# Kernel optimization log

Hardware: AMD Instinct MI355X
Metric: run time of the kernel (lower is better)

## Reference

```python
import jax, jax.numpy as jnp
import numpy as np

BS, D, L, H = 8, 256, 1024, 8
DK = D // H
EPS = 1e-8


def setup_inputs() -> dict:
    key = jax.random.key(0)
    ks = jax.random.split(key, 9)
    queries = jax.random.normal(ks[0], (BS, D, L), jnp.float32)
    keys = jax.random.normal(ks[1], (BS, D, L), jnp.float32)
    values = jax.random.normal(ks[2], (BS, D, L), jnp.float32)
    # binary float mask over positions, (bs, L, 1) as the module expects
    mask = (jax.random.uniform(ks[3], (BS, L, 1)) > 0.1).astype(jnp.float32)
    # grouped 1x1 conv weights: one (dk, dk) block per head (xavier-ish scale)
    wscale = np.sqrt(2.0 / (DK + DK)).astype(np.float32)
    Wq = jax.random.normal(ks[4], (H, DK, DK), jnp.float32) * wscale
    Wk = jax.random.normal(ks[5], (H, DK, DK), jnp.float32) * wscale
    Wv = jax.random.normal(ks[6], (H, DK, DK), jnp.float32) * wscale
    # full 1x1 conv projection
    Wp = jax.random.normal(ks[7], (D, D), jnp.float32) * np.sqrt(1.0 / D).astype(np.float32)
    bp = jnp.zeros((D,), jnp.float32)
    return {"queries": queries, "keys": keys, "values": values, "mask": mask,
            "Wq": Wq, "Wk": Wk, "Wv": Wv, "Wp": Wp, "bp": bp}


def _grouped_conv1x1(x, W):
    # x: (bs, D, L) viewed as (bs, H, dk, L); W: (H, dk_out, dk_in)
    bs, _, l = x.shape
    xh = x.reshape(bs, H, DK, l)
    return jnp.einsum('hij,bhjl->bhil', W, xh)  # (bs, H, dk, L)


def _masked_softmax(logits, mask4):
    # logits: (bs, H, L, L); mask4: (bs, 1, 1, L) -- faithful to module's custom softmax
    max_value = jax.lax.stop_gradient(jnp.max(logits * mask4, axis=-1, keepdims=True))
    z = (logits - max_value) * mask4
    m = jnp.exp(z) * mask4
    n = jnp.sum(m, axis=-1, keepdims=True)
    p_mask = mask4 * jnp.swapaxes(mask4, 2, 3)  # (bs, 1, L, L)
    return p_mask * (m / (n + EPS))


def reference(queries, keys, values, mask, Wq, Wk, Wv, Wp, bp):
    bs, c, l = queries.shape
    m = jnp.swapaxes(mask, 1, 2)          # (bs, 1, L)
    m4 = m[:, :, None, :]                  # (bs, 1, 1, L)
    q = _grouped_conv1x1(queries, Wq) * m4  # (bs, H, dk, L)
    k = _grouped_conv1x1(keys, Wk) * m4
    v = _grouped_conv1x1(values, Wv)
    # attn[b,h,d,e] = sum_c q[b,h,c,d] k[b,h,c,e]  (no 1/sqrt(dk) scaling, as in source)
    attn = jnp.einsum('bhcd,bhce->bhde', q, k)
    atn = _masked_softmax(attn, m4)
    # value[b,h,c,k] = sum_d atn[b,h,k,d] * (v*mask)[b,h,c,d]
    val = jnp.einsum('bhkd,bhcd->bhck', atn, v * m4)
    val = val.reshape(bs, c, l)
    out = jnp.einsum('ij,bjl->bil', Wp, val) + bp[None, :, None]
    return jnp.swapaxes(out * m, 1, 2)      # (bs, L, D)
```

## Files before the change

### kernel.cpp

```cpp
#include <hip/hip_runtime.h>
#include <math.h>


constexpr int cD  = 256;
constexpr int cL  = 1024;
constexpr int cH  = 8;
constexpr int cDK = 32;

typedef _Float16 f16;
typedef __attribute__((ext_vector_type(8))) _Float16 h8;
typedef __attribute__((ext_vector_type(4))) _Float16 h4;
typedef __attribute__((ext_vector_type(4))) float f4v;

__global__ __launch_bounds__(256, 4) void proj_qkv_kernel(
    const float* __restrict__ queries, const float* __restrict__ keys,
    const float* __restrict__ values, const float* __restrict__ mask,
    const float* __restrict__ Wq, const float* __restrict__ Wk,
    const float* __restrict__ Wv, f16* __restrict__ qp_h,
    f16* __restrict__ kp_h, f16* __restrict__ vp_h)
{
    const int t    = threadIdx.x;
    const int bid  = blockIdx.x;
    const int lt   = bid & 15;
    const int bh   = bid >> 4;
    const int h    = bh & 7;
    const int b    = bh >> 3;
    const int l0   = lt * 64;
    const int lane = t & 63, w = t >> 6, ln15 = lane & 15, lq = lane >> 4;
    const int l    = l0 + w * 16 + ln15;

    const float mk = mask[b * cL + l];
    const size_t xbase = ((size_t)(b * cD + h * cDK)) * cL + l;
    const int    wbase = h * cDK * cDK + lq * 8;

    const float* Xs[3] = {queries, keys, values};
    const float* Ws[3] = {Wq, Wk, Wv};
    f4v d0[3], d1[3];

    #pragma unroll
    for (int m = 0; m < 3; ++m) {
        const float* __restrict__ X = Xs[m];
        const float* __restrict__ W = Ws[m];
        h8 bx, a0, a1;
        #pragma unroll
        for (int i = 0; i < 8; ++i)
            bx[i] = (f16)X[xbase + (size_t)(lq * 8 + i) * cL];
        #pragma unroll
        for (int i = 0; i < 8; ++i) {
            a0[i] = (f16)W[wbase + ln15 * cDK + i];
            a1[i] = (f16)W[wbase + (16 + ln15) * cDK + i];
        }
        f4v z = {0.f, 0.f, 0.f, 0.f};
        d0[m] = __builtin_amdgcn_mfma_f32_16x16x32_f16(a0, bx, z, 0, 0, 0);
        d1[m] = __builtin_amdgcn_mfma_f32_16x16x32_f16(a1, bx, z, 0, 0, 0);
    }

    {
        const size_t qb = ((size_t)bh * cL + l) * cDK;
        h4 o0, o1;
        #pragma unroll
        for (int i = 0; i < 4; ++i) { o0[i] = (f16)d0[0][i]; o1[i] = (f16)d1[0][i]; }
        *reinterpret_cast<h4*>(&qp_h[qb + lq * 4])      = o0;
        *reinterpret_cast<h4*>(&qp_h[qb + 16 + lq * 4]) = o1;
    }
    {
        const size_t kb = ((size_t)bh * cL + l) * cDK;
        h4 o0, o1;
        #pragma unroll
        for (int i = 0; i < 4; ++i) {
            o0[i] = (f16)(d0[1][i] * mk);
            o1[i] = (f16)(d1[1][i] * mk);
        }
        *reinterpret_cast<h4*>(&kp_h[kb + lq * 4])      = o0;
        *reinterpret_cast<h4*>(&kp_h[kb + 16 + lq * 4]) = o1;
    }
    {
        const size_t vb = (size_t)bh * cDK * cL + l;
        #pragma unroll
        for (int i = 0; i < 4; ++i) {
            vp_h[vb + (size_t)(lq * 4 + i) * cL]      = (f16)d0[2][i];
            vp_h[vb + (size_t)(16 + lq * 4 + i) * cL] = (f16)d1[2][i];
        }
    }
}

__global__ __launch_bounds__(256, 5) void attn_kernel(
    const float* __restrict__ mask, const f16* __restrict__ qp_h,
    const f16* __restrict__ kp_h, const f16* __restrict__ vp_h,
    f16* __restrict__ val_h)
{
    __shared__ __align__(16) char smem[28672];
    f16* ks  = (f16*)smem;
    f16* vsb = (f16*)(smem + 10240);
    f16* pbf = (f16*)(smem + 19456);

    const int t     = threadIdx.x;
    const int bid   = blockIdx.x;
    const int strip = bid & 15;
    const int bh    = bid >> 4;
    const int b     = bh >> 3;
    const int r0    = strip * 64;
    const int lane  = t & 63;
    const int w     = t >> 6;
    const int ln15  = lane & 15;
    const int lq    = lane >> 4;

    const size_t kvbase = ((size_t)bh) * 32768;
    const int se = t >> 2, sb = (t & 3) * 8;
    const int vc = t >> 3, veb = (t & 7) * 8;

    const h8 qf = *reinterpret_cast<const h8*>(
        &qp_h[((size_t)bh * cL + r0 + w * 16 + ln15) * cDK + lq * 8]);

    {
        h8 kh = *reinterpret_cast<const h8*>(&kp_h[kvbase + se * 32 + sb]);
        *reinterpret_cast<h8*>(&ks[se * 40 + sb]) = kh;
        h8 vv = *reinterpret_cast<const h8*>(&vp_h[kvbase + vc * 1024 + veb]);
        *reinterpret_cast<h8*>(&vsb[vc * 72 + veb]) = vv;
    }

    f4v o0 = {0.f, 0.f, 0.f, 0.f}, o1 = {0.f, 0.f, 0.f, 0.f};
    float mo = -INFINITY, lrp = 0.f;
    const int prow  = (w * 16 + ln15) * 72;
    const int vsoff = ln15 * 72 + lq * 8;

    for (int et = 0; et < 16; ++et) {
        __syncthreads();
        const int pp = et & 1;
        const bool pre = (et < 15);
        h8 khp, vvp;
        if (pre) {
            const int e0n = (et + 1) * 64;
            khp = *reinterpret_cast<const h8*>(&kp_h[kvbase + (e0n + se) * 32 + sb]);
            vvp = *reinterpret_cast<const h8*>(&vp_h[kvbase + vc * 1024 + e0n + veb]);
        }
        float4 mk4[4];
        #pragma unroll
        for (int es = 0; es < 4; ++es)
            mk4[es] = *reinterpret_cast<const float4*>(
                &mask[b * cL + et * 64 + es * 16 + lq * 4]);

        f4v sA[4];
        #pragma unroll
        for (int es = 0; es < 4; ++es) {
            const h8 kf = *reinterpret_cast<const h8*>(
                &ks[pp * 2560 + (es * 16 + ln15) * 40 + lq * 8]);
            f4v z = {0.f, 0.f, 0.f, 0.f};
            sA[es] = __builtin_amdgcn_mfma_f32_16x16x32_f16(kf, qf, z, 0, 0, 0);
        }

        float tm = fmaxf(fmaxf(fmaxf(sA[0][0], sA[0][1]), fmaxf(sA[0][2], sA[0][3])),
                   fmaxf(fmaxf(fmaxf(sA[1][0], sA[1][1]), fmaxf(sA[1][2], sA[1][3])),
                   fmaxf(fmaxf(fmaxf(sA[2][0], sA[2][1]), fmaxf(sA[2][2], sA[2][3])),
                         fmaxf(fmaxf(sA[3][0], sA[3][1]), fmaxf(sA[3][2], sA[3][3])))));
        tm = fmaxf(tm, __shfl_xor(tm, 16));
        tm = fmaxf(tm, __shfl_xor(tm, 32));
        const float mn = fmaxf(mo, tm);
        const float al = __expf(mo - mn);
        mo = mn;
        o0[0] *= al; o0[1] *= al; o0[2] *= al; o0[3] *= al;
        o1[0] *= al; o1[1] *= al; o1[2] *= al; o1[3] *= al;

        float ps = 0.f;
        #pragma unroll
        for (int es = 0; es < 4; ++es) {
            float p0 = mk4[es].x * __expf(sA[es][0] - mn);
            float p1 = mk4[es].y * __expf(sA[es][1] - mn);
            float p2 = mk4[es].z * __expf(sA[es][2] - mn);
            float p3 = mk4[es].w * __expf(sA[es][3] - mn);
            ps += (p0 + p1) + (p2 + p3);
            h4 pk; pk[0] = (f16)p0; pk[1] = (f16)p1; pk[2] = (f16)p2; pk[3] = (f16)p3;
            *reinterpret_cast<h4*>(&pbf[prow + es * 16 + lq * 4]) = pk;
        }
        lrp = lrp * al + ps;

        #pragma unroll
        for (int ch = 0; ch < 2; ++ch) {
            h8 pf  = *reinterpret_cast<const h8*>(&pbf[prow + ch * 32 + lq * 8]);
            h8 va0 = *reinterpret_cast<const h8*>(&vsb[pp * 2304 + vsoff + ch * 32]);
            h8 va1 = *reinterpret_cast<const h8*>(&vsb[pp * 2304 + vsoff + ch * 32 + 1152]);
            o0 = __builtin_amdgcn_mfma_f32_16x16x32_f16(va0, pf, o0, 0, 0, 0);
            o1 = __builtin_amdgcn_mfma_f32_16x16x32_f16(va1, pf, o1, 0, 0, 0);
        }

        if (pre) {
            *reinterpret_cast<h8*>(&ks[(pp ^ 1) * 2560 + se * 40 + sb]) = khp;
            *reinterpret_cast<h8*>(&vsb[(pp ^ 1) * 2304 + vc * 72 + veb]) = vvp;
        }
    }

    {
        float lr = lrp;
        lr += __shfl_xor(lr, 16);
        lr += __shfl_xor(lr, 32);
        const float linv = 1.0f / (lr + 1e-8f);
        const int h = bh & 7;
        const size_t obase = ((size_t)(b * cL + r0 + w * 16 + ln15)) * cD + h * cDK;
        h4 q0, q1;
        #pragma unroll
        for (int i = 0; i < 4; ++i) {
            q0[i] = (f16)(o0[i] * linv);
            q1[i] = (f16)(o1[i] * linv);
        }
        *reinterpret_cast<h4*>(&val_h[obase + lq * 4])      = q0;
        *reinterpret_cast<h4*>(&val_h[obase + 16 + lq * 4]) = q1;
    }
}

__global__ __launch_bounds__(256, 2) void outproj_kernel(
    const f16* __restrict__ val_h, const float* __restrict__ Wp,
    const float* __restrict__ bp, const float* __restrict__ mask,
    float* __restrict__ out)
{
    __shared__ __align__(16) f16 vt[64 * 264];
    __shared__ __align__(16) f16 wpb[64 * 264];
    __shared__ float mrow[64];

    const int t    = threadIdx.x;
    const int bid  = blockIdx.x;
    const int it   = bid & 3;
    const int lt   = (bid >> 2) & 15;
    const int b    = bid >> 6;
    const int l0   = lt * 64, i0 = it * 64;
    const int lane = t & 63, w = t >> 6, ln15 = lane & 15, lq = lane >> 4;

    {
        int row = t & 63, seg = (t >> 6) * 64;
        const f16* src = &val_h[((size_t)(b * cL + l0 + row)) * cD + seg];
        #pragma unroll
        for (int k = 0; k < 8; ++k)
            *reinterpret_cast<h8*>(&vt[row * 264 + seg + k * 8]) =
                *reinterpret_cast<const h8*>(src + k * 8);
    }
    {
        int row = t & 63, seg = (t >> 6) * 64;
        const float* src = &Wp[((size_t)(i0 + row)) * cD + seg];
        #pragma unroll
        for (int k = 0; k < 8; ++k) {
            float4 f0 = *reinterpret_cast<const float4*>(src + k * 8);
            float4 f1 = *reinterpret_cast<const float4*>(src + k * 8 + 4);
            h8 hv;
            hv[0] = (f16)f0.x; hv[1] = (f16)f0.y; hv[2] = (f16)f0.z; hv[3] = (f16)f0.w;
            hv[4] = (f16)f1.x; hv[5] = (f16)f1.y; hv[6] = (f16)f1.z; hv[7] = (f16)f1.w;
            *reinterpret_cast<h8*>(&wpb[row * 264 + seg + k * 8]) = hv;
        }
    }
    if (t < 64) mrow[t] = mask[b * cL + l0 + t];
    __syncthreads();

    f4v acc[4] = {{0.f, 0.f, 0.f, 0.f}, {0.f, 0.f, 0.f, 0.f},
                  {0.f, 0.f, 0.f, 0.f}, {0.f, 0.f, 0.f, 0.f}};
    #pragma unroll
    for (int kc = 0; kc < 8; ++kc) {
        h8 aA = *reinterpret_cast<const h8*>(&vt[(w * 16 + ln15) * 264 + kc * 32 + lq * 8]);
        #pragma unroll
        for (int ti = 0; ti < 4; ++ti) {
            h8 bB = *reinterpret_cast<const h8*>(&wpb[(ti * 16 + ln15) * 264 + kc * 32 + lq * 8]);
            acc[ti] = __builtin_amdgcn_mfma_f32_16x16x32_f16(aA, bB, acc[ti], 0, 0, 0);
        }
    }

    float mk[4];
    #pragma unroll
    for (int rg = 0; rg < 4; ++rg) mk[rg] = mrow[w * 16 + lq * 4 + rg];
    #pragma unroll
    for (int ti = 0; ti < 4; ++ti) {
        float bpv = bp[i0 + ti * 16 + ln15];
        #pragma unroll
        for (int rg = 0; rg < 4; ++rg) {
            int l = l0 + w * 16 + lq * 4 + rg;
            out[((size_t)(b * cL + l)) * cD + i0 + ti * 16 + ln15] =
                (acc[ti][rg] + bpv) * mk[rg];
        }
    }
}

extern "C" void kernel_launch(void* const* d_in, const int* in_sizes, int n_in,
                              void* d_out, int out_size, void* d_ws, size_t ws_size,
                              hipStream_t stream) {
    const float* queries = (const float*)d_in[0];
    const float* keys    = (const float*)d_in[1];
    const float* values  = (const float*)d_in[2];
    const float* mask    = (const float*)d_in[3];
    const float* Wq      = (const float*)d_in[4];
    const float* Wk      = (const float*)d_in[5];
    const float* Wv      = (const float*)d_in[6];
    const float* Wp      = (const float*)d_in[7];
    const float* bp      = (const float*)d_in[8];
    float* out = (float*)d_out;

    char* wsb = (char*)d_ws;
    f16* qp_h  = (f16*)(wsb);
    f16* kp_h  = (f16*)(wsb + (4u << 20));
    f16* vp_h  = (f16*)(wsb + (8u << 20));
    f16* val_h = (f16*)(wsb + (12u << 20));

    proj_qkv_kernel<<<dim3(1024), dim3(256), 0, stream>>>(
        queries, keys, values, mask, Wq, Wk, Wv, qp_h, kp_h, vp_h);
    attn_kernel<<<dim3(1024), dim3(256), 0, stream>>>(
        mask, qp_h, kp_h, vp_h, val_h);
    outproj_kernel<<<dim3(512), dim3(256), 0, stream>>>(val_h, Wp, bp, mask, out);
}
```

Before: 127.3 us.

## Stage projection weights in LDS, pre-convert Wp, use exp2 softmax, reorder attention blocks

The projection kernel now stages each head's fp16 Wq/Wk/Wv in shared memory instead of gathering them per thread from global memory. Extra blocks in the same kernel convert Wp to fp16 once, so the output projection can read val_h and wp_h straight from global memory with no LDS staging and a higher occupancy bound. Q is prescaled by log2(e) so the attention softmax can use exp2f. The attention block index is remapped so consecutive blocks cover different batch-head pairs. The risks are more uncoalesced or repeated global reads in outproj and a small fp16 rounding change from the scaling.

New measurement: 142.1 us. 1.12x slower.

```diff
diff --git a/kernel.cpp b/kernel.cpp
--- a/kernel.cpp
+++ b/kernel.cpp
@@ -6,6 +6,7 @@
 constexpr int cL  = 1024;
 constexpr int cH  = 8;
 constexpr int cDK = 32;
+constexpr float kLog2e = 1.44269504088896f;
 
 typedef _Float16 f16;
 typedef __attribute__((ext_vector_type(8))) _Float16 h8;
@@ -16,11 +17,23 @@
     const float* __restrict__ queries, const float* __restrict__ keys,
     const float* __restrict__ values, const float* __restrict__ mask,
     const float* __restrict__ Wq, const float* __restrict__ Wk,
-    const float* __restrict__ Wv, f16* __restrict__ qp_h,
-    f16* __restrict__ kp_h, f16* __restrict__ vp_h)
+    const float* __restrict__ Wv, const float* __restrict__ Wp,
+    f16* __restrict__ qp_h, f16* __restrict__ kp_h, f16* __restrict__ vp_h,
+    f16* __restrict__ wp_h)
 {
-    const int t    = threadIdx.x;
-    const int bid  = blockIdx.x;
+    const int t   = threadIdx.x;
+    const int bid = blockIdx.x;
+
+    if (bid >= 1024) {
+        const int idx = ((bid - 1024) * 256 + t) * 4;
+        float4 f = *reinterpret_cast<const float4*>(&Wp[idx]);
+        h4 o; o[0] = (f16)f.x; o[1] = (f16)f.y; o[2] = (f16)f.z; o[3] = (f16)f.w;
+        *reinterpret_cast<h4*>(&wp_h[idx]) = o;
+        return;
+    }
+
+    __shared__ __align__(16) f16 wlds[3][32 * 40];
+
     const int lt   = bid & 15;
     const int bh   = bid >> 4;
     const int h    = bh & 7;
@@ -29,27 +42,33 @@
     const int lane = t & 63, w = t >> 6, ln15 = lane & 15, lq = lane >> 4;
     const int l    = l0 + w * 16 + ln15;
 
+    {
+        const float* Wsrc[3] = {Wq, Wk, Wv};
+        const int r = t >> 3, c = (t & 7) * 4;
+        #pragma unroll
+        for (int m = 0; m < 3; ++m) {
+            float4 f = *reinterpret_cast<const float4*>(&Wsrc[m][h * 1024 + t * 4]);
+            h4 o; o[0] = (f16)f.x; o[1] = (f16)f.y; o[2] = (f16)f.z; o[3] = (f16)f.w;
+            *reinterpret_cast<h4*>(&wlds[m][r * 40 + c]) = o;
+        }
+    }
+    __syncthreads();
+
     const float mk = mask[b * cL + l];
     const size_t xbase = ((size_t)(b * cD + h * cDK)) * cL + l;
-    const int    wbase = h * cDK * cDK + lq * 8;
 
     const float* Xs[3] = {queries, keys, values};
-    const float* Ws[3] = {Wq, Wk, Wv};
     f4v d0[3], d1[3];
 
     #pragma unroll
     for (int m = 0; m < 3; ++m) {
         const float* __restrict__ X = Xs[m];
-        const float* __restrict__ W = Ws[m];
-        h8 bx, a0, a1;
+        h8 bx;
         #pragma unroll
         for (int i = 0; i < 8; ++i)
             bx[i] = (f16)X[xbase + (size_t)(lq * 8 + i) * cL];
-        #pragma unroll
-        for (int i = 0; i < 8; ++i) {
-            a0[i] = (f16)W[wbase + ln15 * cDK + i];
-            a1[i] = (f16)W[wbase + (16 + ln15) * cDK + i];
-        }
+        h8 a0 = *reinterpret_cast<const h8*>(&wlds[m][ln15 * 40 + lq * 8]);
+        h8 a1 = *reinterpret_cast<const h8*>(&wlds[m][(16 + ln15) * 40 + lq * 8]);
         f4v z = {0.f, 0.f, 0.f, 0.f};
         d0[m] = __builtin_amdgcn_mfma_f32_16x16x32_f16(a0, bx, z, 0, 0, 0);
         d1[m] = __builtin_amdgcn_mfma_f32_16x16x32_f16(a1, bx, z, 0, 0, 0);
@@ -59,7 +78,10 @@
         const size_t qb = ((size_t)bh * cL + l) * cDK;
         h4 o0, o1;
         #pragma unroll
-        for (int i = 0; i < 4; ++i) { o0[i] = (f16)d0[0][i]; o1[i] = (f16)d1[0][i]; }
+        for (int i = 0; i < 4; ++i) {
+            o0[i] = (f16)(d0[0][i] * kLog2e);
+            o1[i] = (f16)(d1[0][i] * kLog2e);
+        }
         *reinterpret_cast<h4*>(&qp_h[qb + lq * 4])      = o0;
         *reinterpret_cast<h4*>(&qp_h[qb + 16 + lq * 4]) = o1;
     }
@@ -96,8 +118,8 @@
 
     const int t     = threadIdx.x;
     const int bid   = blockIdx.x;
-    const int strip = bid & 15;
-    const int bh    = bid >> 4;
+    const int bh    = bid & 63;
+    const int strip = bid >> 6;
     const int b     = bh >> 3;
     const int r0    = strip * 64;
     const int lane  = t & 63;
@@ -149,14 +171,17 @@
             sA[es] = __builtin_amdgcn_mfma_f32_16x16x32_f16(kf, qf, z, 0, 0, 0);
         }
 
-        float tm = fmaxf(fmaxf(fmaxf(sA[0][0], sA[0][1]), fmaxf(sA[0][2], sA[0][3])),
-                   fmaxf(fmaxf(fmaxf(sA[1][0], sA[1][1]), fmaxf(sA[1][2], sA[1][3])),
-                   fmaxf(fmaxf(fmaxf(sA[2][0], sA[2][1]), fmaxf(sA[2][2], sA[2][3])),
-                         fmaxf(fmaxf(sA[3][0], sA[3][1]), fmaxf(sA[3][2], sA[3][3])))));
+        float tm = -INFINITY;
+        #pragma unroll
+        for (int es = 0; es < 4; ++es) {
+            float r01 = fmaxf(sA[es][0], sA[es][1]);
+            float r23 = fmaxf(sA[es][2], sA[es][3]);
+            tm = fmaxf(tm, fmaxf(r01, r23));
+        }
         tm = fmaxf(tm, __shfl_xor(tm, 16));
         tm = fmaxf(tm, __shfl_xor(tm, 32));
         const float mn = fmaxf(mo, tm);
-        const float al = __expf(mo - mn);
+        const float al = exp2f(mo - mn);
         mo = mn;
         o0[0] *= al; o0[1] *= al; o0[2] *= al; o0[3] *= al;
         o1[0] *= al; o1[1] *= al; o1[2] *= al; o1[3] *= al;
@@ -164,10 +189,10 @@
         float ps = 0.f;
         #pragma unroll
         for (int es = 0; es < 4; ++es) {
-            float p0 = mk4[es].x * __expf(sA[es][0] - mn);
-            float p1 = mk4[es].y * __expf(sA[es][1] - mn);
-            float p2 = mk4[es].z * __expf(sA[es][2] - mn);
-            float p3 = mk4[es].w * __expf(sA[es][3] - mn);
+            float p0 = mk4[es].x * exp2f(sA[es][0] - mn);
+            float p1 = mk4[es].y * exp2f(sA[es][1] - mn);
+            float p2 = mk4[es].z * exp2f(sA[es][2] - mn);
+            float p3 = mk4[es].w * exp2f(sA[es][3] - mn);
             ps += (p0 + p1) + (p2 + p3);
             h4 pk; pk[0] = (f16)p0; pk[1] = (f16)p1; pk[2] = (f16)p2; pk[3] = (f16)p3;
             *reinterpret_cast<h4*>(&pbf[prow + es * 16 + lq * 4]) = pk;
@@ -207,15 +232,11 @@
     }
 }
 
-__global__ __launch_bounds__(256, 2) void outproj_kernel(
-    const f16* __restrict__ val_h, const float* __restrict__ Wp,
+__global__ __launch_bounds__(256, 4) void outproj_kernel(
+    const f16* __restrict__ val_h, const f16* __restrict__ wp_h,
     const float* __restrict__ bp, const float* __restrict__ mask,
     float* __restrict__ out)
 {
-    __shared__ __align__(16) f16 vt[64 * 264];
-    __shared__ __align__(16) f16 wpb[64 * 264];
-    __shared__ float mrow[64];
-
     const int t    = threadIdx.x;
     const int bid  = blockIdx.x;
     const int it   = bid & 3;
@@ -224,45 +245,25 @@
     const int l0   = lt * 64, i0 = it * 64;
     const int lane = t & 63, w = t >> 6, ln15 = lane & 15, lq = lane >> 4;
 
-    {
-        int row = t & 63, seg = (t >> 6) * 64;
-        const f16* src = &val_h[((size_t)(b * cL + l0 + row)) * cD + seg];
-        #pragma unroll
-        for (int k = 0; k < 8; ++k)
-            *reinterpret_cast<h8*>(&vt[row * 264 + seg + k * 8]) =
-                *reinterpret_cast<const h8*>(src + k * 8);
-    }
-    {
-        int row = t & 63, seg = (t >> 6) * 64;
-        const float* src = &Wp[((size_t)(i0 + row)) * cD + seg];
-        #pragma unroll
-        for (int k = 0; k < 8; ++k) {
-            float4 f0 = *reinterpret_cast<const float4*>(src + k * 8);
-            float4 f1 = *reinterpret_cast<const float4*>(src + k * 8 + 4);
-            h8 hv;
-            hv[0] = (f16)f0.x; hv[1] = (f16)f0.y; hv[2] = (f16)f0.z; hv[3] = (f16)f0.w;
-            hv[4] = (f16)f1.x; hv[5] = (f16)f1.y; hv[6] = (f16)f1.z; hv[7] = (f16)f1.w;
-            *reinterpret_cast<h8*>(&wpb[row * 264 + seg + k * 8]) = hv;
-        }
-    }
-    if (t < 64) mrow[t] = mask[b * cL + l0 + t];
-    __syncthreads();
+    const size_t abase = ((size_t)(b * cL + l0 + w * 16 + ln15)) * cD + lq * 8;
 
     f4v acc[4] = {{0.f, 0.f, 0.f, 0.f}, {0.f, 0.f, 0.f, 0.f},
                   {0.f, 0.f, 0.f, 0.f}, {0.f, 0.f, 0.f, 0.f}};
     #pragma unroll
     for (int kc = 0; kc < 8; ++kc) {
-        h8 aA = *reinterpret_cast<const h8*>(&vt[(w * 16 + ln15) * 264 + kc * 32 + lq * 8]);
+        h8 aA = *reinterpret_cast<const h8*>(&val_h[abase + kc * 32]);
         #pragma unroll
         for (int ti = 0; ti < 4; ++ti) {
-            h8 bB = *reinterpret_cast<const h8*>(&wpb[(ti * 16 + ln15) * 264 + kc * 32 + lq * 8]);
+            h8 bB = *reinterpret_cast<const h8*>(
+                &wp_h[((size_t)(i0 + ti * 16 + ln15)) * cD + kc * 32 + lq * 8]);
             acc[ti] = __builtin_amdgcn_mfma_f32_16x16x32_f16(aA, bB, acc[ti], 0, 0, 0);
         }
     }
 
     float mk[4];
     #pragma unroll
-    for (int rg = 0; rg < 4; ++rg) mk[rg] = mrow[w * 16 + lq * 4 + rg];
+    for (int rg = 0; rg < 4; ++rg)
+        mk[rg] = mask[b * cL + l0 + w * 16 + lq * 4 + rg];
     #pragma unroll
     for (int ti = 0; ti < 4; ++ti) {
         float bpv = bp[i0 + ti * 16 + ln15];
@@ -294,10 +295,11 @@
     f16* kp_h  = (f16*)(wsb + (4u << 20));
     f16* vp_h  = (f16*)(wsb + (8u << 20));
     f16* val_h = (f16*)(wsb + (12u << 20));
-
-    proj_qkv_kernel<<<dim3(1024), dim3(256), 0, stream>>>(
-        queries, keys, values, mask, Wq, Wk, Wv, qp_h, kp_h, vp_h);
+    f16* wp_h  = (f16*)(wsb + (16u << 20));
+
+    proj_qkv_kernel<<<dim3(1088), dim3(256), 0, stream>>>(
+        queries, keys, values, mask, Wq, Wk, Wv, Wp, qp_h, kp_h, vp_h, wp_h);
     attn_kernel<<<dim3(1024), dim3(256), 0, stream>>>(
         mask, qp_h, kp_h, vp_h, val_h);
-    outproj_kernel<<<dim3(512), dim3(256), 0, stream>>>(val_h, Wp, bp, mask, out);
+    outproj_kernel<<<dim3(512), dim3(256), 0, stream>>>(val_h, wp_h, bp, mask, out);
 }
```
